# Kernel optimization log

Hardware: AMD Instinct MI355X
Metric: run time of the kernel (lower is better)

Reference implementation:

```python
import jax, jax.numpy as jnp
import numpy as np

GRAPH_BIAS_SCALE = 0.8
COMMITMENT_COST = 0.01

B, S, L, N = 4, 2048, 512, 8192
D = 2 * L  # codebook feature dim


def setup_inputs() -> dict:
    key = jax.random.key(0)
    ks = jax.random.split(key, 9)
    gw_real = jax.random.normal(ks[0], (B, S, L), dtype=jnp.float32)
    gw_imag = jax.random.normal(ks[1], (B, S, L), dtype=jnp.float32)
    prev_symbol_idx = jax.random.randint(ks[2], (B, S), 0, N)
    codebook = jax.random.uniform(ks[3], (N, D), jnp.float32, -0.5, 0.5)
    adjacency = 0.1 * jax.random.normal(ks[4], (N, N), dtype=jnp.float32)
    sal_w = 0.02 * jax.random.normal(ks[5], (D, 1), dtype=jnp.float32)
    sal_b = jnp.zeros((1,), jnp.float32)
    conf_w = 0.02 * jax.random.normal(ks[6], (D, 1), dtype=jnp.float32)
    conf_b = jnp.zeros((1,), jnp.float32)
    return dict(gw_real=gw_real, gw_imag=gw_imag, prev_symbol_idx=prev_symbol_idx,
                codebook=codebook, adjacency=adjacency,
                sal_w=sal_w, sal_b=sal_b, conf_w=conf_w, conf_b=conf_b)


def reference(gw_real, gw_imag, prev_symbol_idx, codebook, adjacency,
              sal_w, sal_b, conf_w, conf_b):
    sg = jax.lax.stop_gradient
    # z_flat = cat(real, imag): [B, S, D]
    z = jnp.concatenate([gw_real, gw_imag], axis=-1)
    # squared euclidean distances to codebook: [B, S, N]
    d = (jnp.sum(z * z, axis=-1, keepdims=True)
         + jnp.sum(codebook * codebook, axis=-1)
         - 2.0 * jnp.einsum('bsd,nd->bsn', z, codebook))
    # graph prior bias from adjacency rows of previous symbols
    graph_prior = adjacency[prev_symbol_idx]            # [B, S, N]
    d = d - GRAPH_BIAS_SCALE * jax.nn.sigmoid(graph_prior)
    min_indices = jnp.argmin(d, axis=-1)                # [B, S]
    z_q = codebook[min_indices]                         # [B, S, D]
    loss_vq = jnp.mean((z_q - sg(z)) ** 2)
    loss_commit = jnp.mean((sg(z_q) - z) ** 2)
    # straight-through estimator
    z_q_st = z + sg(z_q - z)
    dist_score = -jnp.min(d, axis=-1, keepdims=True)    # [B, S, 1]
    salience = z_q_st @ sal_w + sal_b + 0.1 * dist_score
    confidence = jax.nn.sigmoid(z_q_st @ conf_w + conf_b)
    total_loss = loss_vq + COMMITMENT_COST * loss_commit
    proposal_real = z_q_st[..., :L]
    proposal_imag = z_q_st[..., L:]
    return (proposal_real, proposal_imag, salience, confidence, total_loss, min_indices)
```

## Files before the change

kernel.cpp:

```cpp
#include <hip/hip_runtime.h>
#include <math.h>

#define RDIM 8192
#define DDIM 1024
#define NDIM 8192
#define LDIM 512
#define KT 16

#define OFF_REAL 0
#define OFF_IMAG 4194304
#define OFF_SAL  8388608
#define OFF_CONF 8396800
#define OFF_LOSS 8404992
#define OFF_IDX  8404993

#define MAXCAND 64
#define MARGIN_Q 76
#define QSCALE 64.0f
#define FLT_BIG 3.4e38f

typedef __attribute__((ext_vector_type(8))) short bf16x8;
typedef __attribute__((ext_vector_type(8))) short short8v;
typedef __attribute__((ext_vector_type(4))) float f32x4;

__device__ __forceinline__ unsigned short f2bf(float x) {
  unsigned u = __builtin_bit_cast(unsigned, x);
  unsigned r = (u + 0x7fff + ((u >> 16) & 1)) >> 16;
  return (unsigned short)r;
}

__device__ __forceinline__ void load_lds16(const void* g, void* l) {
  __builtin_amdgcn_global_load_lds((const __attribute__((address_space(1))) void*)g,
                                   (__attribute__((address_space(3))) void*)l, 16, 0, 0);
}

__device__ __forceinline__ int qbias(float s) {
  int qi = __float2int_rn(s * QSCALE);
  qi = qi > 32767 ? 32767 : (qi < -32767 ? -32767 : qi);
  return qi + 32768;
}

__global__ __launch_bounds__(256)
void split_norms_kernel(const float* __restrict__ gw_real, const float* __restrict__ gw_imag,
                        const float* __restrict__ codebook,
                        unsigned short* __restrict__ zh, unsigned short* __restrict__ ch,
                        float* __restrict__ znorm, float* __restrict__ cnorm) {
  const int w = threadIdx.x >> 6, l = threadIdx.x & 63;
  const int id = blockIdx.x * 4 + w;
  const float* src;
  unsigned short* dst;
  float* nrm;
  int row;
  if (id < RDIM) {
    row = id; dst = zh; nrm = znorm;
    src = (l < 32) ? gw_real + (size_t)row * LDIM + l * 16
                   : gw_imag + (size_t)row * LDIM + (l - 32) * 16;
  } else {
    row = id - RDIM; dst = ch; nrm = cnorm;
    src = codebook + (size_t)row * DDIM + l * 16;
  }
  float f[16];
#pragma unroll
  for (int i = 0; i < 4; ++i) {
    const float4 v = reinterpret_cast<const float4*>(src)[i];
    f[i*4+0] = v.x; f[i*4+1] = v.y; f[i*4+2] = v.z; f[i*4+3] = v.w;
  }
  short8v h0, h1;
  float s = 0.f;
#pragma unroll
  for (int i = 0; i < 8; ++i) { h0[i] = (short)f2bf(f[i]);     s += f[i] * f[i]; }
#pragma unroll
  for (int i = 0; i < 8; ++i) { h1[i] = (short)f2bf(f[8 + i]); s += f[8+i] * f[8+i]; }
  unsigned short* dp = dst + (size_t)row * DDIM + l * 16;
  *reinterpret_cast<short8v*>(dp)     = h0;
  *reinterpret_cast<short8v*>(dp + 8) = h1;
#pragma unroll
  for (int m = 1; m < 64; m <<= 1) s += __shfl_xor(s, m, 64);
  if (l == 0) nrm[row] = s;
}

#define STAGE(basep, kt, ldsbyte) do {                                        \
    load_lds16((basep) + eo1 + (kt) * 64, L + (ldsbyte) + wid * 1024);        \
    load_lds16((basep) + eo2 + (kt) * 64, L + (ldsbyte) + 8192 + wid * 1024); \
  } while (0)

__global__ __launch_bounds__(512)
void dist_mfma_kernel(const unsigned short* __restrict__ zh, const unsigned short* __restrict__ ch,
                      const float* __restrict__ cnorm,
                      unsigned* __restrict__ keys, unsigned long long* __restrict__ masks) {
  __shared__ unsigned short ldsbuf[65536];
  char* const L = (char*)ldsbuf;

  const int sidx = (int)blockIdx.x;
  const int sw = (sidx & 7) * 128 + (sidx >> 3);
  const int bm = sw >> 5, bn = sw & 31;
  const int row0 = bm * 256, col0 = bn * 256;

  const int tid = threadIdx.x;
  const int wid = tid >> 6, l = tid & 63;
  const int wm = wid >> 2, wn = wid & 3;
  const int lr = l & 15, lg = l >> 4;

  const int p1 = tid, p2 = tid + 512;
  const int r1 = p1 >> 3, c1 = (p1 & 7) ^ (r1 & 7);
  const int r2 = p2 >> 3, c2 = (p2 & 7) ^ (r2 & 7);
  const int eo1 = r1 * DDIM + c1 * 8;
  const int eo2 = r2 * DDIM + c2 * 8;
  const unsigned short* const az0 = zh + (size_t)row0 * DDIM;
  const unsigned short* const az1 = zh + (size_t)(row0 + 128) * DDIM;
  const unsigned short* const ac0 = ch + (size_t)col0 * DDIM;
  const unsigned short* const ac1 = ch + (size_t)(col0 + 128) * DDIM;

  const int fo0 = lr * 128 + ((lg ^ (lr & 7)) << 4);
  const int fo1 = fo0 ^ 64;

  f32x4 acc[4][8];
#pragma unroll
  for (int i = 0; i < 4; ++i)
#pragma unroll
    for (int j = 0; j < 8; ++j)
      acc[i][j] = (f32x4){0.f, 0.f, 0.f, 0.f};

  bf16x8 cfA[2][2], cfB[2][2], zf[4][2];

  STAGE(az0, 0, 0);
  STAGE(az1, 0, 16384);
  STAGE(ac0, 0, 32768);
  STAGE(ac1, 0, 49152);
  STAGE(ac0, 1, 98304);
  STAGE(ac1, 1, 114688);
  asm volatile("s_waitcnt vmcnt(4)" ::: "memory");
  __builtin_amdgcn_sched_barrier(0);
  __builtin_amdgcn_s_barrier();

  for (int t = 0; t < KT; ++t) {
    const int buf = t & 1, nbuf = buf ^ 1;
    const char* const Ab = L + buf * 65536 + wm * 16384;
    const char* const Bb = L + buf * 65536 + 32768 + wn * 8192;

#pragma unroll
    for (int i = 0; i < 2; ++i) {
      cfA[i][0] = *reinterpret_cast<const bf16x8*>(Bb + i * 2048 + fo0);
      cfA[i][1] = *reinterpret_cast<const bf16x8*>(Bb + i * 2048 + fo1);
    }
#pragma unroll
    for (int j = 0; j < 4; ++j) {
      zf[j][0] = *reinterpret_cast<const bf16x8*>(Ab + j * 2048 + fo0);
      zf[j][1] = *reinterpret_cast<const bf16x8*>(Ab + j * 2048 + fo1);
    }
    if (t + 1 < KT) STAGE(az0, t + 1, nbuf * 65536);
    __builtin_amdgcn_sched_barrier(0);
    __builtin_amdgcn_s_barrier();
    __builtin_amdgcn_s_setprio(1);
#pragma unroll
    for (int kh = 0; kh < 2; ++kh)
#pragma unroll
      for (int i = 0; i < 2; ++i)
#pragma unroll
        for (int j = 0; j < 4; ++j)
          acc[i][j] = __builtin_amdgcn_mfma_f32_16x16x32_bf16(cfA[i][kh], zf[j][kh], acc[i][j], 0, 0, 0);
    __builtin_amdgcn_s_setprio(0);
    __builtin_amdgcn_sched_barrier(0);
    __builtin_amdgcn_s_barrier();

#pragma unroll
    for (int i = 0; i < 2; ++i) {
      cfB[i][0] = *reinterpret_cast<const bf16x8*>(Bb + (2 + i) * 2048 + fo0);
      cfB[i][1] = *reinterpret_cast<const bf16x8*>(Bb + (2 + i) * 2048 + fo1);
    }
    if (t + 1 < KT) STAGE(az1, t + 1, nbuf * 65536 + 16384);
    __builtin_amdgcn_sched_barrier(0);
    __builtin_amdgcn_s_barrier();
    __builtin_amdgcn_s_setprio(1);
#pragma unroll
    for (int kh = 0; kh < 2; ++kh)
#pragma unroll
      for (int i = 0; i < 2; ++i)
#pragma unroll
        for (int j = 0; j < 4; ++j)
          acc[2 + i][j] = __builtin_amdgcn_mfma_f32_16x16x32_bf16(cfB[i][kh], zf[j][kh], acc[2 + i][j], 0, 0, 0);
    __builtin_amdgcn_s_setprio(0);
    __builtin_amdgcn_sched_barrier(0);
    __builtin_amdgcn_s_barrier();

#pragma unroll
    for (int j = 0; j < 4; ++j) {
      zf[j][0] = *reinterpret_cast<const bf16x8*>(Ab + (4 + j) * 2048 + fo0);
      zf[j][1] = *reinterpret_cast<const bf16x8*>(Ab + (4 + j) * 2048 + fo1);
    }
    if (t + 2 < KT) STAGE(ac0, t + 2, buf * 65536 + 32768);
    __builtin_amdgcn_sched_barrier(0);
    __builtin_amdgcn_s_barrier();
    __builtin_amdgcn_s_setprio(1);
#pragma unroll
    for (int kh = 0; kh < 2; ++kh)
#pragma unroll
      for (int i = 0; i < 2; ++i)
#pragma unroll
        for (int j = 0; j < 4; ++j)
          acc[2 + i][4 + j] = __builtin_amdgcn_mfma_f32_16x16x32_bf16(cfB[i][kh], zf[j][kh], acc[2 + i][4 + j], 0, 0, 0);
    __builtin_amdgcn_s_setprio(0);
    __builtin_amdgcn_sched_barrier(0);
    __builtin_amdgcn_s_barrier();

    if (t + 2 < KT) STAGE(ac1, t + 2, buf * 65536 + 49152);
    if (t < KT - 2) { asm volatile("s_waitcnt vmcnt(4)" ::: "memory"); }
    else            { asm volatile("s_waitcnt vmcnt(0)" ::: "memory"); }
    __builtin_amdgcn_sched_barrier(0);
    __builtin_amdgcn_s_barrier();
    __builtin_amdgcn_s_setprio(1);
#pragma unroll
    for (int kh = 0; kh < 2; ++kh)
#pragma unroll
      for (int i = 0; i < 2; ++i)
#pragma unroll
        for (int j = 0; j < 4; ++j)
          acc[i][4 + j] = __builtin_amdgcn_mfma_f32_16x16x32_bf16(cfA[i][kh], zf[j][kh], acc[i][4 + j], 0, 0, 0);
    __builtin_amdgcn_s_setprio(0);
    __builtin_amdgcn_sched_barrier(0);
    __builtin_amdgcn_s_barrier();
  }

  const int czero = col0 + wn * 64;
  const int zzero = row0 + wm * 128;
  const int slice = bn * 4 + wn;
  float cnv[4][4];
#pragma unroll
  for (int i = 0; i < 4; ++i) {
    const float4 c4 = *reinterpret_cast<const float4*>(cnorm + czero + i * 16 + lg * 4);
    cnv[i][0] = c4.x; cnv[i][1] = c4.y; cnv[i][2] = c4.z; cnv[i][3] = c4.w;
  }
#pragma unroll
  for (int j = 0; j < 8; ++j) {
    const int row = zzero + j * 16 + lr;
    int qv[16];
    unsigned kmin = 0xffffffffu;
#pragma unroll
    for (int i = 0; i < 4; ++i)
#pragma unroll
      for (int reg = 0; reg < 4; ++reg) {
        const int col = czero + i * 16 + lg * 4 + reg;
        const int qb = qbias(cnv[i][reg] - 2.0f * acc[i][j][reg]);
        qv[i * 4 + reg] = qb;
        const unsigned key = ((unsigned)qb << 13) | (unsigned)col;
        kmin = key < kmin ? key : kmin;
      }
    {
      unsigned o = (unsigned)__shfl_xor((int)kmin, 16, 64);
      kmin = o < kmin ? o : kmin;
      o = (unsigned)__shfl_xor((int)kmin, 32, 64);
      kmin = o < kmin ? o : kmin;
    }
    const int thr = (int)(kmin >> 13) + MARGIN_Q;
    unsigned mlo = 0, mhi = 0;
#pragma unroll
    for (int i = 0; i < 4; ++i) {
      unsigned nib = 0;
#pragma unroll
      for (int reg = 0; reg < 4; ++reg)
        if (qv[i * 4 + reg] <= thr) nib |= 1u << reg;
      const int sh = i * 16 + lg * 4;
      if (i < 2) mlo |= nib << sh;
      else       mhi |= nib << (sh - 32);
    }
    mlo |= (unsigned)__shfl_xor((int)mlo, 16, 64);
    mlo |= (unsigned)__shfl_xor((int)mlo, 32, 64);
    mhi |= (unsigned)__shfl_xor((int)mhi, 16, 64);
    mhi |= (unsigned)__shfl_xor((int)mhi, 32, 64);
    if (lg == 0) {
      keys[(size_t)slice * RDIM + row] = kmin;
      masks[(size_t)slice * RDIM + row] = ((unsigned long long)mhi << 32) | (unsigned long long)mlo;
    }
  }
}

__global__ __launch_bounds__(64)
void collect_refine_kernel(const unsigned* __restrict__ keys,
                           const unsigned long long* __restrict__ masks,
                           const int* __restrict__ prev, const float* __restrict__ adj,
                           const float* __restrict__ gw_real, const float* __restrict__ gw_imag,
                           const float* __restrict__ codebook,
                           const float* __restrict__ znorm, const float* __restrict__ cnorm,
                           float* __restrict__ out, float* __restrict__ minfinal,
                           int* __restrict__ idxfinal) {
  __shared__ int s_list[MAXCAND];
  __shared__ int s_cnt;
  const int row = blockIdx.x;
  const int t = threadIdx.x;
  if (t == 0) s_cnt = 0;
  __syncthreads();
  const unsigned k0 = keys[(size_t)(2 * t) * RDIM + row];
  const unsigned k1 = keys[(size_t)(2 * t + 1) * RDIM + row];
  unsigned kmin = k0 < k1 ? k0 : k1;
#pragma unroll
  for (int m = 1; m < 64; m <<= 1) {
    const unsigned o = (unsigned)__shfl_xor((int)kmin, m, 64);
    kmin = o < kmin ? o : kmin;
  }
  const int qmin_b = (int)(kmin >> 13);
  const int winner = (int)(kmin & 8191u);
  const int thr = qmin_b + MARGIN_Q;
#pragma unroll
  for (int s2 = 0; s2 < 2; ++s2) {
    const int s = 2 * t + s2;
    const unsigned key = s2 ? k1 : k0;
    if ((int)(key >> 13) <= thr) {
      unsigned long long m = masks[(size_t)s * RDIM + row];
      while (m) {
        const int b = __builtin_ctzll(m);
        m &= m - 1;
        const int pos = atomicAdd(&s_cnt, 1);
        if (pos < MAXCAND) s_list[pos] = s * 64 + b;
      }
    }
  }
  __syncthreads();
  const int cnt = (s_cnt < MAXCAND) ? s_cnt : MAXCAND;
  if (cnt <= 1) {
    if (t == 0) {
      const int p = prev[row];
      const float bias = 0.8f / (1.0f + expf(-adj[(size_t)p * NDIM + winner]));
      out[OFF_IDX + row] = (float)winner;
      idxfinal[row] = winner;
      minfinal[row] = znorm[row] + (float)(qmin_b - 32768) * (1.0f / QSCALE) - bias;
    }
    return;
  }
  const int base = t * 16;
  const float* zp = (base < LDIM) ? gw_real + (size_t)row * LDIM + base
                                  : gw_imag + (size_t)row * LDIM + (base - LDIM);
  float z[16];
#pragma unroll
  for (int c = 0; c < 4; ++c) {
    const float4 zv = reinterpret_cast<const float4*>(zp)[c];
    z[c*4+0] = zv.x; z[c*4+1] = zv.y; z[c*4+2] = zv.z; z[c*4+3] = zv.w;
  }
  const float zn = znorm[row];
  const int p = prev[row];
  float bestd = FLT_BIG;
  int besti = 0x7fffffff;
  for (int j = 0; j < cnt; ++j) {
    const int idx = s_list[j];
    const float* cp = codebook + (size_t)idx * DDIM + base;
    float dot = 0.f;
#pragma unroll
    for (int c = 0; c < 4; ++c) {
      const float4 cv = reinterpret_cast<const float4*>(cp)[c];
      dot += z[c*4+0]*cv.x + z[c*4+1]*cv.y + z[c*4+2]*cv.z + z[c*4+3]*cv.w;
    }
    for (int m = 1; m < 64; m <<= 1) dot += __shfl_xor(dot, m, 64);
    const float d = zn + cnorm[idx] - 2.0f * dot
                  - 0.8f / (1.0f + expf(-adj[(size_t)p * NDIM + idx]));
    if (d < bestd || (d == bestd && idx < besti)) { bestd = d; besti = idx; }
  }
  if (t == 0) {
    out[OFF_IDX + row] = (float)besti;
    minfinal[row] = bestd;
    idxfinal[row] = besti;
  }
}


__global__ __launch_bounds__(256)
void epilogue_kernel(const float* __restrict__ gw_real, const float* __restrict__ gw_imag,
                     const float* __restrict__ codebook,
                     const float* __restrict__ sal_w, const float* __restrict__ sal_b,
                     const float* __restrict__ conf_w, const float* __restrict__ conf_b,
                     const float* __restrict__ minfinal, const int* __restrict__ idxfinal,
                     float* __restrict__ out, float* __restrict__ rowloss) {
  __shared__ float s1[4], s2[4], s3[4];
  const int row = blockIdx.x;
  const int t = threadIdx.x;
  const int w = t >> 6, l = t & 63;
  const int k = t << 2;
  const int idx = idxfinal[row];
  const float4 qv = *reinterpret_cast<const float4*>(codebook + (size_t)idx * DDIM + k);
  float4 z;
  if (k < LDIM) z = *reinterpret_cast<const float4*>(gw_real + (size_t)row * LDIM + k);
  else          z = *reinterpret_cast<const float4*>(gw_imag + (size_t)row * LDIM + (k - LDIM));
  const float dx = qv.x - z.x, dy = qv.y - z.y, dz = qv.z - z.z, dw = qv.w - z.w;
  float4 st;
  st.x = z.x + dx; st.y = z.y + dy; st.z = z.z + dz; st.w = z.w + dw;
  float* dst = (k < LDIM) ? (out + OFF_REAL + (size_t)row * LDIM + k)
                          : (out + OFF_IMAG + (size_t)row * LDIM + (k - LDIM));
  *reinterpret_cast<float4*>(dst) = st;
  const float4 sw = *reinterpret_cast<const float4*>(sal_w + k);
  const float4 cw = *reinterpret_cast<const float4*>(conf_w + k);
  float r1 = st.x*sw.x + st.y*sw.y + st.z*sw.z + st.w*sw.w;
  float r2 = st.x*cw.x + st.y*cw.y + st.z*cw.z + st.w*cw.w;
  float r3 = dx*dx + dy*dy + dz*dz + dw*dw;
#pragma unroll
  for (int m = 1; m < 64; m <<= 1) {
    r1 += __shfl_xor(r1, m, 64);
    r2 += __shfl_xor(r2, m, 64);
    r3 += __shfl_xor(r3, m, 64);
  }
  if (l == 0) { s1[w] = r1; s2[w] = r2; s3[w] = r3; }
  __syncthreads();
  if (t == 0) {
    const float t1 = s1[0] + s1[1] + s1[2] + s1[3];
    const float t2 = s2[0] + s2[1] + s2[2] + s2[3];
    const float t3 = s3[0] + s3[1] + s3[2] + s3[3];
    out[OFF_SAL + row]  = t1 + sal_b[0] + 0.1f * (-minfinal[row]);
    out[OFF_CONF + row] = 1.0f / (1.0f + expf(-(t2 + conf_b[0])));
    rowloss[row] = t3;
  }
}

__global__ __launch_bounds__(256)
void loss_kernel(const float* __restrict__ rowloss, float* __restrict__ out) {
  const int t = threadIdx.x;
  float s = 0.f;
  for (int i = t; i < RDIM; i += 256) s += rowloss[i];
  __shared__ float red[256];
  red[t] = s;
  __syncthreads();
  for (int st = 128; st > 0; st >>= 1) {
    if (t < st) red[t] += red[t + st];
    __syncthreads();
  }
  if (t == 0) {
    const float m = red[0] / (float)((size_t)RDIM * DDIM);
    out[OFF_LOSS] = m + 0.01f * m;
  }
}


__global__ __launch_bounds__(256)
void norms_kernel(const float* __restrict__ gw_real, const float* __restrict__ gw_imag,
                  const float* __restrict__ codebook,
                  float* __restrict__ znorm, float* __restrict__ cnorm) {
  const int id = blockIdx.x;
  const int t = threadIdx.x;
  float s;
  if (id < RDIM) {
    const float4* zr = reinterpret_cast<const float4*>(gw_real + (size_t)id * LDIM);
    const float4* zi = reinterpret_cast<const float4*>(gw_imag + (size_t)id * LDIM);
    const float4 v = (t < 128) ? zr[t] : zi[t - 128];
    s = v.x*v.x + v.y*v.y + v.z*v.z + v.w*v.w;
  } else {
    const float4* c = reinterpret_cast<const float4*>(codebook + (size_t)(id - RDIM) * DDIM);
    const float4 v = c[t];
    s = v.x*v.x + v.y*v.y + v.z*v.z + v.w*v.w;
  }
  __shared__ float red[256];
  red[t] = s;
  __syncthreads();
  for (int st = 128; st > 0; st >>= 1) {
    if (t < st) red[t] += red[t + st];
    __syncthreads();
  }
  if (t == 0) {
    if (id < RDIM) znorm[id] = red[0];
    else           cnorm[id - RDIM] = red[0];
  }
}

__global__ __launch_bounds__(256)
void dist_kernel(const float* __restrict__ gw_real, const float* __restrict__ gw_imag,
                 const float* __restrict__ codebook, const int* __restrict__ prev,
                 const float* __restrict__ adj, const float* __restrict__ znorm,
                 const float* __restrict__ cnorm,
                 float* __restrict__ ws_min, int* __restrict__ ws_idx) {
  __shared__ float As[16][64];
  __shared__ float Bs[16][64];
  __shared__ int prevs[64];
  const int bm = blockIdx.x, bn = blockIdx.y;
  const int row0 = bm * 64, col0 = bn * 64;
  const int tid = threadIdx.x;
  const int tx = tid & 15, ty = tid >> 4;
  if (tid < 64) prevs[tid] = prev[row0 + tid];
  const int lm = tid >> 2;
  const int lk = (tid & 3) << 2;
  const int arow = row0 + lm;
  const int brow = col0 + lm;
  float acc[4][4] = {{0.f,0.f,0.f,0.f},{0.f,0.f,0.f,0.f},{0.f,0.f,0.f,0.f},{0.f,0.f,0.f,0.f}};
  for (int kk = 0; kk < DDIM; kk += 16) {
    const int k = kk + lk;
    float4 a, b;
    if (k < LDIM) a = *reinterpret_cast<const float4*>(gw_real + (size_t)arow * LDIM + k);
    else          a = *reinterpret_cast<const float4*>(gw_imag + (size_t)arow * LDIM + (k - LDIM));
    b = *reinterpret_cast<const float4*>(codebook + (size_t)brow * DDIM + k);
    __syncthreads();
    As[lk+0][lm]=a.x; As[lk+1][lm]=a.y; As[lk+2][lm]=a.z; As[lk+3][lm]=a.w;
    Bs[lk+0][lm]=b.x; Bs[lk+1][lm]=b.y; Bs[lk+2][lm]=b.z; Bs[lk+3][lm]=b.w;
    __syncthreads();
#pragma unroll
    for (int k2 = 0; k2 < 16; ++k2) {
      const float4 a4 = *reinterpret_cast<const float4*>(&As[k2][ty << 2]);
      const float4 b4 = *reinterpret_cast<const float4*>(&Bs[k2][tx << 2]);
      const float av[4] = {a4.x, a4.y, a4.z, a4.w};
      const float bv[4] = {b4.x, b4.y, b4.z, b4.w};
#pragma unroll
      for (int i = 0; i < 4; ++i)
#pragma unroll
        for (int j = 0; j < 4; ++j)
          acc[i][j] = fmaf(av[i], bv[j], acc[i][j]);
    }
  }
  const float4 cn4 = *reinterpret_cast<const float4*>(cnorm + col0 + (tx << 2));
  const float cnv[4] = {cn4.x, cn4.y, cn4.z, cn4.w};
#pragma unroll
  for (int i = 0; i < 4; ++i) {
    const int rsub = (ty << 2) + i;
    const int row = row0 + rsub;
    const float zn = znorm[row];
    const int p = prevs[rsub];
    const float4 ad4 = *reinterpret_cast<const float4*>(adj + (size_t)p * NDIM + col0 + (tx << 2));
    const float adv[4] = {ad4.x, ad4.y, ad4.z, ad4.w};
    float bv = FLT_BIG;
    int bi = -1;
#pragma unroll
    for (int j = 0; j < 4; ++j) {
      const float bias = 0.8f * (1.0f / (1.0f + expf(-adv[j])));
      const float dv = (zn + cnv[j]) - 2.0f * acc[i][j] - bias;
      const int col = col0 + (tx << 2) + j;
      if (dv < bv) { bv = dv; bi = col; }
    }
    for (int m = 1; m < 16; m <<= 1) {
      const float ov = __shfl_xor(bv, m, 64);
      const int   oi = __shfl_xor(bi, m, 64);
      if (ov < bv || (ov == bv && oi < bi)) { bv = ov; bi = oi; }
    }
    if (tx == 0) {
      ws_min[(size_t)row * 128 + bn] = bv;
      ws_idx[(size_t)row * 128 + bn] = bi;
    }
  }
}

__global__ __launch_bounds__(128)
void argmin_reduce(const float* __restrict__ ws_min, const int* __restrict__ ws_idx,
                   float* __restrict__ out, float* __restrict__ minfinal,
                   int* __restrict__ idxfinal) {
  const int row = blockIdx.x;
  const int t = threadIdx.x;
  __shared__ float sv[128];
  __shared__ int   si[128];
  sv[t] = ws_min[(size_t)row * 128 + t];
  si[t] = ws_idx[(size_t)row * 128 + t];
  __syncthreads();
  for (int s = 64; s > 0; s >>= 1) {
    if (t < s) {
      const float ov = sv[t + s];
      const int   oi = si[t + s];
      if (ov < sv[t] || (ov == sv[t] && oi < si[t])) { sv[t] = ov; si[t] = oi; }
    }
    __syncthreads();
  }
  if (t == 0) {
    out[OFF_IDX + row] = (float)si[0];
    minfinal[row] = sv[0];
    idxfinal[row] = si[0];
  }
}


extern "C" void kernel_launch(void* const* d_in, const int* in_sizes, int n_in,
                              void* d_out, int out_size, void* d_ws, size_t ws_size,
                              hipStream_t stream) {
  const float* gw_real  = (const float*)d_in[0];
  const float* gw_imag  = (const float*)d_in[1];
  const int*   prev     = (const int*)d_in[2];
  const float* codebook = (const float*)d_in[3];
  const float* adj      = (const float*)d_in[4];
  const float* sal_w    = (const float*)d_in[5];
  const float* sal_b    = (const float*)d_in[6];
  const float* conf_w   = (const float*)d_in[7];
  const float* conf_b   = (const float*)d_in[8];
  float* out = (float*)d_out;
  char* ws = (char*)d_ws;

  const size_t matsz  = (size_t)RDIM * DDIM;
  const size_t nslice = (size_t)RDIM * 128;
  size_t need = 2 * matsz * 2
              + nslice * 4 + nslice * 8
              + 5 * (size_t)RDIM * 4 + 4096;

  if (ws_size >= need) {
    unsigned short* zh = (unsigned short*)ws;
    unsigned short* chh = zh + matsz;
    unsigned* keys = (unsigned*)(chh + matsz);
    unsigned long long* masks = (unsigned long long*)(keys + nslice);
    float* znorm    = (float*)(masks + nslice);
    float* cnorm    = znorm + RDIM;
    float* minfinal = cnorm + NDIM;
    int*   idxfinal = (int*)(minfinal + RDIM);
    float* rowloss  = (float*)(idxfinal + RDIM);

    split_norms_kernel<<<(RDIM + NDIM) / 4, 256, 0, stream>>>(gw_real, gw_imag, codebook,
                                                              zh, chh, znorm, cnorm);
    dist_mfma_kernel<<<1024, 512, 0, stream>>>(zh, chh, cnorm, keys, masks);
    collect_refine_kernel<<<RDIM, 64, 0, stream>>>(keys, masks, prev, adj,
                                                   gw_real, gw_imag, codebook,
                                                   znorm, cnorm, out, minfinal, idxfinal);
    epilogue_kernel<<<RDIM, 256, 0, stream>>>(gw_real, gw_imag, codebook, sal_w, sal_b,
                                              conf_w, conf_b, minfinal, idxfinal, out, rowloss);
    loss_kernel<<<1, 256, 0, stream>>>(rowloss, out);
  } else {
    float* ws_min   = (float*)ws;
    int*   ws_idx   = (int*)(ws + (size_t)RDIM * 128 * 4);
    float* znorm    = (float*)(ws + (size_t)RDIM * 128 * 8);
    float* cnorm    = znorm + RDIM;
    float* minfinal = cnorm + NDIM;
    int*   idxfinal = (int*)(minfinal + RDIM);
    float* rowloss  = (float*)(idxfinal + RDIM);

    norms_kernel<<<RDIM + NDIM, 256, 0, stream>>>(gw_real, gw_imag, codebook, znorm, cnorm);
    dist_kernel<<<dim3(RDIM / 64, NDIM / 64), 256, 0, stream>>>(
        gw_real, gw_imag, codebook, prev, adj, znorm, cnorm, ws_min, ws_idx);
    argmin_reduce<<<RDIM, 128, 0, stream>>>(ws_min, ws_idx, out, minfinal, idxfinal);
    epilogue_kernel<<<RDIM, 256, 0, stream>>>(gw_real, gw_imag, codebook, sal_w, sal_b,
                                              conf_w, conf_b, minfinal, idxfinal, out, rowloss);
    loss_kernel<<<1, 256, 0, stream>>>(rowloss, out);
  }
}
```

Baseline: 195.3 us.

## Fuse candidate refine and epilogue into one tail kernel; drop sched barriers

Merges collect_refine_kernel and epilogue_kernel into a single 256-thread tail_kernel. It refines the candidate list across four waves, reduces the winner in shared memory, then writes the proposal, salience, confidence and row loss directly. This removes a kernel launch and the minfinal/idxfinal round trip through global memory. Separately, it removes the sched_barrier(0) calls in the MFMA main loop, so the compiler can reorder LDS loads and MFMAs around the s_barriers. That may help or hurt the hand-tuned interleaving.

```diff
diff --git a/kernel.cpp b/kernel.cpp
--- a/kernel.cpp
+++ b/kernel.cpp
@@ -130,7 +130,6 @@
   STAGE(ac0, 1, 98304);
   STAGE(ac1, 1, 114688);
   asm volatile("s_waitcnt vmcnt(4)" ::: "memory");
-  __builtin_amdgcn_sched_barrier(0);
   __builtin_amdgcn_s_barrier();
 
   for (int t = 0; t < KT; ++t) {
@@ -149,7 +148,6 @@
       zf[j][1] = *reinterpret_cast<const bf16x8*>(Ab + j * 2048 + fo1);
     }
     if (t + 1 < KT) STAGE(az0, t + 1, nbuf * 65536);
-    __builtin_amdgcn_sched_barrier(0);
     __builtin_amdgcn_s_barrier();
     __builtin_amdgcn_s_setprio(1);
 #pragma unroll
@@ -160,7 +158,6 @@
         for (int j = 0; j < 4; ++j)
           acc[i][j] = __builtin_amdgcn_mfma_f32_16x16x32_bf16(cfA[i][kh], zf[j][kh], acc[i][j], 0, 0, 0);
     __builtin_amdgcn_s_setprio(0);
-    __builtin_amdgcn_sched_barrier(0);
     __builtin_amdgcn_s_barrier();
 
 #pragma unroll
@@ -169,7 +166,6 @@
       cfB[i][1] = *reinterpret_cast<const bf16x8*>(Bb + (2 + i) * 2048 + fo1);
     }
     if (t + 1 < KT) STAGE(az1, t + 1, nbuf * 65536 + 16384);
-    __builtin_amdgcn_sched_barrier(0);
     __builtin_amdgcn_s_barrier();
     __builtin_amdgcn_s_setprio(1);
 #pragma unroll
@@ -180,7 +176,6 @@
         for (int j = 0; j < 4; ++j)
           acc[2 + i][j] = __builtin_amdgcn_mfma_f32_16x16x32_bf16(cfB[i][kh], zf[j][kh], acc[2 + i][j], 0, 0, 0);
     __builtin_amdgcn_s_setprio(0);
-    __builtin_amdgcn_sched_barrier(0);
     __builtin_amdgcn_s_barrier();
 
 #pragma unroll
@@ -189,7 +184,6 @@
       zf[j][1] = *reinterpret_cast<const bf16x8*>(Ab + (4 + j) * 2048 + fo1);
     }
     if (t + 2 < KT) STAGE(ac0, t + 2, buf * 65536 + 32768);
-    __builtin_amdgcn_sched_barrier(0);
     __builtin_amdgcn_s_barrier();
     __builtin_amdgcn_s_setprio(1);
 #pragma unroll
@@ -200,13 +194,11 @@
         for (int j = 0; j < 4; ++j)
           acc[2 + i][4 + j] = __builtin_amdgcn_mfma_f32_16x16x32_bf16(cfB[i][kh], zf[j][kh], acc[2 + i][4 + j], 0, 0, 0);
     __builtin_amdgcn_s_setprio(0);
-    __builtin_amdgcn_sched_barrier(0);
     __builtin_amdgcn_s_barrier();
 
     if (t + 2 < KT) STAGE(ac1, t + 2, buf * 65536 + 49152);
     if (t < KT - 2) { asm volatile("s_waitcnt vmcnt(4)" ::: "memory"); }
     else            { asm volatile("s_waitcnt vmcnt(0)" ::: "memory"); }
-    __builtin_amdgcn_sched_barrier(0);
     __builtin_amdgcn_s_barrier();
     __builtin_amdgcn_s_setprio(1);
 #pragma unroll
@@ -217,7 +209,6 @@
         for (int j = 0; j < 4; ++j)
           acc[i][4 + j] = __builtin_amdgcn_mfma_f32_16x16x32_bf16(cfA[i][kh], zf[j][kh], acc[i][4 + j], 0, 0, 0);
     __builtin_amdgcn_s_setprio(0);
-    __builtin_amdgcn_sched_barrier(0);
     __builtin_amdgcn_s_barrier();
   }
 
@@ -274,120 +265,116 @@
   }
 }
 
-__global__ __launch_bounds__(64)
-void collect_refine_kernel(const unsigned* __restrict__ keys,
-                           const unsigned long long* __restrict__ masks,
-                           const int* __restrict__ prev, const float* __restrict__ adj,
-                           const float* __restrict__ gw_real, const float* __restrict__ gw_imag,
-                           const float* __restrict__ codebook,
-                           const float* __restrict__ znorm, const float* __restrict__ cnorm,
-                           float* __restrict__ out, float* __restrict__ minfinal,
-                           int* __restrict__ idxfinal) {
+__global__ __launch_bounds__(256)
+void tail_kernel(const unsigned* __restrict__ keys, const unsigned long long* __restrict__ masks,
+                 const int* __restrict__ prev, const float* __restrict__ adj,
+                 const float* __restrict__ gw_real, const float* __restrict__ gw_imag,
+                 const float* __restrict__ codebook,
+                 const float* __restrict__ sal_w, const float* __restrict__ sal_b,
+                 const float* __restrict__ conf_w, const float* __restrict__ conf_b,
+                 const float* __restrict__ znorm, const float* __restrict__ cnorm,
+                 float* __restrict__ out, float* __restrict__ rowloss) {
+  __shared__ unsigned s_wmin[4];
+  __shared__ int s_cnt;
   __shared__ int s_list[MAXCAND];
-  __shared__ int s_cnt;
-  const int row = blockIdx.x;
-  const int t = threadIdx.x;
-  if (t == 0) s_cnt = 0;
-  __syncthreads();
-  const unsigned k0 = keys[(size_t)(2 * t) * RDIM + row];
-  const unsigned k1 = keys[(size_t)(2 * t + 1) * RDIM + row];
-  unsigned kmin = k0 < k1 ? k0 : k1;
-#pragma unroll
-  for (int m = 1; m < 64; m <<= 1) {
-    const unsigned o = (unsigned)__shfl_xor((int)kmin, m, 64);
-    kmin = o < kmin ? o : kmin;
-  }
-  const int qmin_b = (int)(kmin >> 13);
-  const int winner = (int)(kmin & 8191u);
-  const int thr = qmin_b + MARGIN_Q;
-#pragma unroll
-  for (int s2 = 0; s2 < 2; ++s2) {
-    const int s = 2 * t + s2;
-    const unsigned key = s2 ? k1 : k0;
-    if ((int)(key >> 13) <= thr) {
-      unsigned long long m = masks[(size_t)s * RDIM + row];
-      while (m) {
-        const int b = __builtin_ctzll(m);
-        m &= m - 1;
-        const int pos = atomicAdd(&s_cnt, 1);
-        if (pos < MAXCAND) s_list[pos] = s * 64 + b;
-      }
-    }
-  }
-  __syncthreads();
-  const int cnt = (s_cnt < MAXCAND) ? s_cnt : MAXCAND;
-  if (cnt <= 1) {
-    if (t == 0) {
-      const int p = prev[row];
-      const float bias = 0.8f / (1.0f + expf(-adj[(size_t)p * NDIM + winner]));
-      out[OFF_IDX + row] = (float)winner;
-      idxfinal[row] = winner;
-      minfinal[row] = znorm[row] + (float)(qmin_b - 32768) * (1.0f / QSCALE) - bias;
-    }
-    return;
-  }
-  const int base = t * 16;
-  const float* zp = (base < LDIM) ? gw_real + (size_t)row * LDIM + base
-                                  : gw_imag + (size_t)row * LDIM + (base - LDIM);
-  float z[16];
-#pragma unroll
-  for (int c = 0; c < 4; ++c) {
-    const float4 zv = reinterpret_cast<const float4*>(zp)[c];
-    z[c*4+0] = zv.x; z[c*4+1] = zv.y; z[c*4+2] = zv.z; z[c*4+3] = zv.w;
-  }
-  const float zn = znorm[row];
-  const int p = prev[row];
-  float bestd = FLT_BIG;
-  int besti = 0x7fffffff;
-  for (int j = 0; j < cnt; ++j) {
-    const int idx = s_list[j];
-    const float* cp = codebook + (size_t)idx * DDIM + base;
-    float dot = 0.f;
-#pragma unroll
-    for (int c = 0; c < 4; ++c) {
-      const float4 cv = reinterpret_cast<const float4*>(cp)[c];
-      dot += z[c*4+0]*cv.x + z[c*4+1]*cv.y + z[c*4+2]*cv.z + z[c*4+3]*cv.w;
-    }
-    for (int m = 1; m < 64; m <<= 1) dot += __shfl_xor(dot, m, 64);
-    const float d = zn + cnorm[idx] - 2.0f * dot
-                  - 0.8f / (1.0f + expf(-adj[(size_t)p * NDIM + idx]));
-    if (d < bestd || (d == bestd && idx < besti)) { bestd = d; besti = idx; }
-  }
-  if (t == 0) {
-    out[OFF_IDX + row] = (float)besti;
-    minfinal[row] = bestd;
-    idxfinal[row] = besti;
-  }
-}
-
-
-__global__ __launch_bounds__(256)
-void epilogue_kernel(const float* __restrict__ gw_real, const float* __restrict__ gw_imag,
-                     const float* __restrict__ codebook,
-                     const float* __restrict__ sal_w, const float* __restrict__ sal_b,
-                     const float* __restrict__ conf_w, const float* __restrict__ conf_b,
-                     const float* __restrict__ minfinal, const int* __restrict__ idxfinal,
-                     float* __restrict__ out, float* __restrict__ rowloss) {
+  __shared__ float s_bv[4], s_fd;
+  __shared__ int   s_bi[4], s_fi;
   __shared__ float s1[4], s2[4], s3[4];
   const int row = blockIdx.x;
   const int t = threadIdx.x;
   const int w = t >> 6, l = t & 63;
-  const int k = t << 2;
-  const int idx = idxfinal[row];
-  const float4 qv = *reinterpret_cast<const float4*>(codebook + (size_t)idx * DDIM + k);
-  float4 z;
-  if (k < LDIM) z = *reinterpret_cast<const float4*>(gw_real + (size_t)row * LDIM + k);
-  else          z = *reinterpret_cast<const float4*>(gw_imag + (size_t)row * LDIM + (k - LDIM));
-  const float dx = qv.x - z.x, dy = qv.y - z.y, dz = qv.z - z.z, dw = qv.w - z.w;
+  if (t == 0) s_cnt = 0;
+  const unsigned k = (t < 128) ? keys[(size_t)t * RDIM + row] : 0xffffffffu;
+  unsigned km = k;
+#pragma unroll
+  for (int m = 1; m < 64; m <<= 1) {
+    const unsigned o = (unsigned)__shfl_xor((int)km, m, 64);
+    km = o < km ? o : km;
+  }
+  if (l == 0) s_wmin[w] = km;
+  __syncthreads();
+  unsigned gk = s_wmin[0];
+  gk = gk < s_wmin[1] ? gk : s_wmin[1];
+  gk = gk < s_wmin[2] ? gk : s_wmin[2];
+  gk = gk < s_wmin[3] ? gk : s_wmin[3];
+  const int qmin_b = (int)(gk >> 13);
+  const int winner = (int)(gk & 8191u);
+  const int thr = qmin_b + MARGIN_Q;
+  if (t < 128 && (int)(k >> 13) <= thr) {
+    unsigned long long m = masks[(size_t)t * RDIM + row];
+    while (m) {
+      const int b = __builtin_ctzll(m);
+      m &= m - 1;
+      const int pos = atomicAdd(&s_cnt, 1);
+      if (pos < MAXCAND) s_list[pos] = t * 64 + b;
+    }
+  }
+  __syncthreads();
+  const int cnt = (s_cnt < MAXCAND) ? s_cnt : MAXCAND;
+  const float zn = znorm[row];
+  const int p = prev[row];
+  if (cnt <= 1) {
+    if (t == 0) {
+      const float bias = 0.8f / (1.0f + expf(-adj[(size_t)p * NDIM + winner]));
+      s_fi = winner;
+      s_fd = zn + (float)(qmin_b - 32768) * (1.0f / QSCALE) - bias;
+    }
+  } else {
+    const int base = l * 16;
+    const float* zp = (base < LDIM) ? gw_real + (size_t)row * LDIM + base
+                                    : gw_imag + (size_t)row * LDIM + (base - LDIM);
+    float z[16];
+#pragma unroll
+    for (int c = 0; c < 4; ++c) {
+      const float4 zv = reinterpret_cast<const float4*>(zp)[c];
+      z[c*4+0] = zv.x; z[c*4+1] = zv.y; z[c*4+2] = zv.z; z[c*4+3] = zv.w;
+    }
+    float bestd = FLT_BIG;
+    int besti = 0x7fffffff;
+    for (int j = w; j < cnt; j += 4) {
+      const int idx = s_list[j];
+      const float* cp = codebook + (size_t)idx * DDIM + base;
+      float dot = 0.f;
+#pragma unroll
+      for (int c = 0; c < 4; ++c) {
+        const float4 cv = reinterpret_cast<const float4*>(cp)[c];
+        dot += z[c*4+0]*cv.x + z[c*4+1]*cv.y + z[c*4+2]*cv.z + z[c*4+3]*cv.w;
+      }
+      for (int m = 1; m < 64; m <<= 1) dot += __shfl_xor(dot, m, 64);
+      const float d = zn + cnorm[idx] - 2.0f * dot
+                    - 0.8f / (1.0f + expf(-adj[(size_t)p * NDIM + idx]));
+      if (d < bestd || (d == bestd && idx < besti)) { bestd = d; besti = idx; }
+    }
+    if (l == 0) { s_bv[w] = bestd; s_bi[w] = besti; }
+    __syncthreads();
+    if (t == 0) {
+      float bv = s_bv[0]; int bi = s_bi[0];
+#pragma unroll
+      for (int w2 = 1; w2 < 4; ++w2) {
+        const float ov = s_bv[w2]; const int oi = s_bi[w2];
+        if (ov < bv || (ov == bv && oi < bi)) { bv = ov; bi = oi; }
+      }
+      s_fd = bv; s_fi = bi;
+    }
+  }
+  __syncthreads();
+  const int idx = s_fi;
+  const float dmin = s_fd;
+  const int k4 = t << 2;
+  const float4 qv = *reinterpret_cast<const float4*>(codebook + (size_t)idx * DDIM + k4);
+  float4 z4;
+  if (k4 < LDIM) z4 = *reinterpret_cast<const float4*>(gw_real + (size_t)row * LDIM + k4);
+  else           z4 = *reinterpret_cast<const float4*>(gw_imag + (size_t)row * LDIM + (k4 - LDIM));
+  const float dx = qv.x - z4.x, dy = qv.y - z4.y, dz = qv.z - z4.z, dw = qv.w - z4.w;
   float4 st;
-  st.x = z.x + dx; st.y = z.y + dy; st.z = z.z + dz; st.w = z.w + dw;
-  float* dst = (k < LDIM) ? (out + OFF_REAL + (size_t)row * LDIM + k)
-                          : (out + OFF_IMAG + (size_t)row * LDIM + (k - LDIM));
+  st.x = z4.x + dx; st.y = z4.y + dy; st.z = z4.z + dz; st.w = z4.w + dw;
+  float* dst = (k4 < LDIM) ? (out + OFF_REAL + (size_t)row * LDIM + k4)
+                           : (out + OFF_IMAG + (size_t)row * LDIM + (k4 - LDIM));
   *reinterpret_cast<float4*>(dst) = st;
-  const float4 sw = *reinterpret_cast<const float4*>(sal_w + k);
-  const float4 cw = *reinterpret_cast<const float4*>(conf_w + k);
-  float r1 = st.x*sw.x + st.y*sw.y + st.z*sw.z + st.w*sw.w;
-  float r2 = st.x*cw.x + st.y*cw.y + st.z*cw.z + st.w*cw.w;
+  const float4 sw4 = *reinterpret_cast<const float4*>(sal_w + k4);
+  const float4 cw4 = *reinterpret_cast<const float4*>(conf_w + k4);
+  float r1 = st.x*sw4.x + st.y*sw4.y + st.z*sw4.z + st.w*sw4.w;
+  float r2 = st.x*cw4.x + st.y*cw4.y + st.z*cw4.z + st.w*cw4.w;
   float r3 = dx*dx + dy*dy + dz*dz + dw*dw;
 #pragma unroll
   for (int m = 1; m < 64; m <<= 1) {
@@ -401,7 +388,8 @@
     const float t1 = s1[0] + s1[1] + s1[2] + s1[3];
     const float t2 = s2[0] + s2[1] + s2[2] + s2[3];
     const float t3 = s3[0] + s3[1] + s3[2] + s3[3];
-    out[OFF_SAL + row]  = t1 + sal_b[0] + 0.1f * (-minfinal[row]);
+    out[OFF_IDX + row] = (float)idx;
+    out[OFF_SAL + row]  = t1 + sal_b[0] + 0.1f * (-dmin);
     out[OFF_CONF + row] = 1.0f / (1.0f + expf(-(t2 + conf_b[0])));
     rowloss[row] = t3;
   }
@@ -555,6 +543,52 @@
   }
 }
 
+__global__ __launch_bounds__(256)
+void epilogue_kernel(const float* __restrict__ gw_real, const float* __restrict__ gw_imag,
+                     const float* __restrict__ codebook,
+                     const float* __restrict__ sal_w, const float* __restrict__ sal_b,
+                     const float* __restrict__ conf_w, const float* __restrict__ conf_b,
+                     const float* __restrict__ minfinal, const int* __restrict__ idxfinal,
+                     float* __restrict__ out, float* __restrict__ rowloss) {
+  __shared__ float s1[4], s2[4], s3[4];
+  const int row = blockIdx.x;
+  const int t = threadIdx.x;
+  const int w = t >> 6, l = t & 63;
+  const int k = t << 2;
+  const int idx = idxfinal[row];
+  const float4 qv = *reinterpret_cast<const float4*>(codebook + (size_t)idx * DDIM + k);
+  float4 z;
+  if (k < LDIM) z = *reinterpret_cast<const float4*>(gw_real + (size_t)row * LDIM + k);
+  else          z = *reinterpret_cast<const float4*>(gw_imag + (size_t)row * LDIM + (k - LDIM));
+  const float dx = qv.x - z.x, dy = qv.y - z.y, dz = qv.z - z.z, dw = qv.w - z.w;
+  float4 st;
+  st.x = z.x + dx; st.y = z.y + dy; st.z = z.z + dz; st.w = z.w + dw;
+  float* dst = (k < LDIM) ? (out + OFF_REAL + (size_t)row * LDIM + k)
+                          : (out + OFF_IMAG + (size_t)row * LDIM + (k - LDIM));
+  *reinterpret_cast<float4*>(dst) = st;
+  const float4 sw = *reinterpret_cast<const float4*>(sal_w + k);
+  const float4 cw = *reinterpret_cast<const float4*>(conf_w + k);
+  float r1 = st.x*sw.x + st.y*sw.y + st.z*sw.z + st.w*sw.w;
+  float r2 = st.x*cw.x + st.y*cw.y + st.z*cw.z + st.w*cw.w;
+  float r3 = dx*dx + dy*dy + dz*dz + dw*dw;
+#pragma unroll
+  for (int m = 1; m < 64; m <<= 1) {
+    r1 += __shfl_xor(r1, m, 64);
+    r2 += __shfl_xor(r2, m, 64);
+    r3 += __shfl_xor(r3, m, 64);
+  }
+  if (l == 0) { s1[w] = r1; s2[w] = r2; s3[w] = r3; }
+  __syncthreads();
+  if (t == 0) {
+    const float t1 = s1[0] + s1[1] + s1[2] + s1[3];
+    const float t2 = s2[0] + s2[1] + s2[2] + s2[3];
+    const float t3 = s3[0] + s3[1] + s3[2] + s3[3];
+    out[OFF_SAL + row]  = t1 + sal_b[0] + 0.1f * (-minfinal[row]);
+    out[OFF_CONF + row] = 1.0f / (1.0f + expf(-(t2 + conf_b[0])));
+    rowloss[row] = t3;
+  }
+}
+
 
 extern "C" void kernel_launch(void* const* d_in, const int* in_sizes, int n_in,
                               void* d_out, int out_size, void* d_ws, size_t ws_size,
@@ -584,18 +618,14 @@
     unsigned long long* masks = (unsigned long long*)(keys + nslice);
     float* znorm    = (float*)(masks + nslice);
     float* cnorm    = znorm + RDIM;
-    float* minfinal = cnorm + NDIM;
-    int*   idxfinal = (int*)(minfinal + RDIM);
-    float* rowloss  = (float*)(idxfinal + RDIM);
+    float* rowloss  = cnorm + NDIM;
 
     split_norms_kernel<<<(RDIM + NDIM) / 4, 256, 0, stream>>>(gw_real, gw_imag, codebook,
                                                               zh, chh, znorm, cnorm);
     dist_mfma_kernel<<<1024, 512, 0, stream>>>(zh, chh, cnorm, keys, masks);
-    collect_refine_kernel<<<RDIM, 64, 0, stream>>>(keys, masks, prev, adj,
-                                                   gw_real, gw_imag, codebook,
-                                                   znorm, cnorm, out, minfinal, idxfinal);
-    epilogue_kernel<<<RDIM, 256, 0, stream>>>(gw_real, gw_imag, codebook, sal_w, sal_b,
-                                              conf_w, conf_b, minfinal, idxfinal, out, rowloss);
+    tail_kernel<<<RDIM, 256, 0, stream>>>(keys, masks, prev, adj, gw_real, gw_imag, codebook,
+                                          sal_w, sal_b, conf_w, conf_b, znorm, cnorm,
+                                          out, rowloss);
     loss_kernel<<<1, 256, 0, stream>>>(rowloss, out);
   } else {
     float* ws_min   = (float*)ws;
```

New measurement: 190.4 us. 2.5% less time.
